# Kernel optimization log

Hardware: AMD Instinct MI355X
Metric: run time of the kernel (lower is better)

The kernel has to match this reference:

```python
import jax, jax.numpy as jnp
import numpy as np

E = 500000          # num edges
N = 50000           # num nodes
D_IN = 32           # n_input_features (edge feature dim)
D_HID = 128         # n_hidden_features
D_NODE = 16         # n_node_features; MLP head outputs D_NODE**2


def _linear_params(key, d_in, d_out):
    kw, kb = jax.random.split(key)
    bound = 1.0 / np.sqrt(d_in)
    W = jax.random.uniform(kw, (d_out, d_in), jnp.float32, -bound, bound)
    b = jax.random.uniform(kb, (d_out,), jnp.float32, -bound, bound)
    return W, b


def setup_inputs() -> dict:
    key = jax.random.key(0)
    k1, k2, k3, k4, k5, k6, k7 = jax.random.split(key, 7)
    edge_features = jax.random.normal(k1, (E, D_IN), jnp.float32)
    node_features = jax.random.normal(k2, (N, D_NODE), jnp.float32)
    edge_index = jax.random.randint(k3, (E, 2), 0, N, jnp.int64 if jax.config.jax_enable_x64 else jnp.int32)
    W1, b1 = _linear_params(k4, D_IN, D_HID)
    W2, b2 = _linear_params(k5, D_HID, D_HID)
    W3, b3 = _linear_params(k6, D_HID, D_HID)
    W4, b4 = _linear_params(k7, D_HID, D_NODE * D_NODE)
    return {
        "edge_features": edge_features,
        "node_features": node_features,
        "W1": W1, "b1": b1, "W2": W2, "b2": b2,
        "W3": W3, "b3": b3, "W4": W4, "b4": b4,
        "edge_index": edge_index,
    }


def reference(edge_features, node_features, W1, b1, W2, b2, W3, b3, W4, b4, edge_index):
    neighbors = edge_index[:, 1]                       # [E]
    ef = edge_features[neighbors]                      # [E, D_IN] gather
    nf = node_features[neighbors]                      # [E, D_NODE] gather
    h = jax.nn.relu(ef @ W1.T + b1)                    # [E, D_HID]
    h = jax.nn.relu(h @ W2.T + b2)
    h = jax.nn.relu(h @ W3.T + b3)
    edge_out = h @ W4.T + b4                           # [E, D_NODE**2]
    d = nf.shape[-1]
    message = edge_out.reshape(-1, d, d)               # [E, d, d]
    # per-edge matrix-vector product: (message @ nf[..., None]).squeeze(-1)
    return jnp.einsum("eij,ej->ei", message, nf)       # [E, d]
```

## Files before the change

kernel.cpp:

```cpp
#include <hip/hip_runtime.h>
#include <stdint.h>

typedef __attribute__((ext_vector_type(8))) short short8;
typedef __attribute__((ext_vector_type(4))) float f32x4;
typedef __attribute__((ext_vector_type(4))) unsigned int u32x4;

#define NE 500000
#define NN 50000
#define NTILES 3125
#define WSLOTS 2048
#define SC_BLOCKS 2048
#define SC_THREADS (SC_BLOCKS * 256)

__device__ __forceinline__ unsigned int f2bf1(float f) {
  unsigned int u = __builtin_bit_cast(unsigned int, f);
  u += 0x7FFFu + ((u >> 16) & 1u);
  return u >> 16;
}
__device__ __forceinline__ unsigned int packbf2(float lo, float hi) {
  return f2bf1(lo) | (f2bf1(hi) << 16);
}
__device__ __forceinline__ short8 pack8(f32x4 a, f32x4 b) {
  short8 r;
  r[0] = (short)f2bf1(a[0]); r[1] = (short)f2bf1(a[1]);
  r[2] = (short)f2bf1(a[2]); r[3] = (short)f2bf1(a[3]);
  r[4] = (short)f2bf1(b[0]); r[5] = (short)f2bf1(b[1]);
  r[6] = (short)f2bf1(b[2]); r[7] = (short)f2bf1(b[3]);
  return r;
}

__global__ __launch_bounds__(256) void prep_weights(
    const float* __restrict__ W1, const float* __restrict__ W2,
    const float* __restrict__ W3, const float* __restrict__ W4,
    unsigned short* __restrict__ wf) {
  int idx = blockIdx.x * 256 + threadIdx.x;
  if (idx >= 8704) return;
  int f = idx >> 6, l = idx & 63;
  int c2 = l & 15, g = l >> 4;
  const float *pa, *pb;
  if (f < 8) {
    const float* base = W1 + (f * 16 + c2) * 32 + g * 8;
    pa = base; pb = base + 4;
  } else {
    const float* W; int i2, kfq, nb;
    if (f < 40)      { W = W2; i2 = f - 8;  kfq = i2 >> 3; nb = i2 & 7;  }
    else if (f < 72) { W = W3; i2 = f - 40; kfq = i2 >> 3; nb = i2 & 7;  }
    else             { W = W4; i2 = f - 72; kfq = i2 >> 4; nb = i2 & 15; }
    const float* base = W + (nb * 16 + c2) * 128 + g * 4;
    pa = base + kfq * 16;
    pb = base + (kfq + 4) * 16;
  }
  f32x4 x0 = *(const f32x4*)pa;
  f32x4 x1 = *(const f32x4*)pb;
  *(short8*)&wf[f * 512 + l * 8] = pack8(x0, x1);
}

__global__ __launch_bounds__(512, 2) void mlp_kernel(
    const float* __restrict__ ef, const float* __restrict__ nfeat,
    const float* __restrict__ b1, const float* __restrict__ b2,
    const float* __restrict__ b3, const float* __restrict__ b4,
    const unsigned short* __restrict__ wf, float* __restrict__ Rout) {
  __shared__ __align__(16) unsigned short wlds[69632];
  __shared__ __align__(16) float blds[640];

  const int t = threadIdx.x;
  {
    const u32x4* src = (const u32x4*)wf;
    u32x4* dst = (u32x4*)wlds;
    #pragma unroll
    for (int i = 0; i < 17; ++i) dst[t + i * 512] = src[t + i * 512];
  }
  if (t < 160) {
    const float* s = t < 32 ? b1 + t * 4
                   : t < 64 ? b2 + (t - 32) * 4
                   : t < 96 ? b3 + (t - 64) * 4
                   :          b4 + (t - 96) * 4;
    ((f32x4*)blds)[t] = *(const f32x4*)s;
  }
  __syncthreads();

  const int lane = t & 63, w = t >> 6;
  const int l15 = lane & 15, lg = lane >> 4;

  const int g = w * 256 + blockIdx.x;
  const int tA = g;
  const bool actB = (g + WSLOTS < NTILES);
  const int tB = actB ? g + WSLOTS : g;
  const int nA = tA * 16, nB = tB * 16;

  auto transition = [&](const f32x4* a, short8* af) {
    unsigned int pk[8][2];
    #pragma unroll
    for (int nb = 0; nb < 8; ++nb) {
      pk[nb][0] = packbf2(fmaxf(a[nb][0], 0.f), fmaxf(a[nb][1], 0.f));
      pk[nb][1] = packbf2(fmaxf(a[nb][2], 0.f), fmaxf(a[nb][3], 0.f));
    }
    #pragma unroll
    for (int kf = 0; kf < 4; ++kf) {
      u32x4 u = { pk[kf][0], pk[kf][1], pk[kf + 4][0], pk[kf + 4][1] };
      af[kf] = __builtin_bit_cast(short8, u);
    }
  };

  const float* xa = ef + (nA + l15) * 32 + lg * 8;
  const float* xb = ef + (nB + l15) * 32 + lg * 8;
  short8 a1A = pack8(*(const f32x4*)xa, *(const f32x4*)(xa + 4));
  short8 a1B = pack8(*(const f32x4*)xb, *(const f32x4*)(xb + 4));
  f32x4 accA[8], accB[8];
  #pragma unroll
  for (int nb = 0; nb < 8; ++nb) {
    f32x4 c0 = *(const f32x4*)&blds[nb * 16 + lg * 4];
    short8 wv = *(const short8*)&wlds[nb * 512 + lane * 8];
    accA[nb] = __builtin_amdgcn_mfma_f32_16x16x32_bf16(wv, a1A, c0, 0, 0, 0);
    accB[nb] = __builtin_amdgcn_mfma_f32_16x16x32_bf16(wv, a1B, c0, 0, 0, 0);
  }
  short8 afA[4], afB[4];
  transition(accA, afA);
  transition(accB, afB);

  #pragma unroll
  for (int L = 0; L < 2; ++L) {
    const int wbase = 8 + L * 32, bbase = 128 + L * 128;
    #pragma unroll
    for (int nb = 0; nb < 8; ++nb) {
      f32x4 c0 = *(const f32x4*)&blds[bbase + nb * 16 + lg * 4];
      f32x4 cA = c0, cB = c0;
      #pragma unroll
      for (int kf = 0; kf < 4; ++kf) {
        short8 wv = *(const short8*)&wlds[(wbase + kf * 8 + nb) * 512 + lane * 8];
        cA = __builtin_amdgcn_mfma_f32_16x16x32_bf16(wv, afA[kf], cA, 0, 0, 0);
        cB = __builtin_amdgcn_mfma_f32_16x16x32_bf16(wv, afB[kf], cB, 0, 0, 0);
      }
      accA[nb] = cA; accB[nb] = cB;
    }
    transition(accA, afA);
    transition(accB, afB);
  }

  f32x4 nfvA = *(const f32x4*)(nfeat + (nA + l15) * 16 + lg * 4);
  f32x4 nfvB = *(const f32x4*)(nfeat + (nB + l15) * 16 + lg * 4);
  float oA0 = 0.f, oA1 = 0.f, oA2 = 0.f, oA3 = 0.f;
  float oB0 = 0.f, oB1 = 0.f, oB2 = 0.f, oB3 = 0.f;
  #pragma unroll
  for (int nb = 0; nb < 16; ++nb) {
    f32x4 c0 = *(const f32x4*)&blds[384 + nb * 16 + lg * 4];
    f32x4 dA = c0, dB = c0;
    #pragma unroll
    for (int kf = 0; kf < 4; ++kf) {
      short8 wv = *(const short8*)&wlds[(72 + kf * 16 + nb) * 512 + lane * 8];
      dA = __builtin_amdgcn_mfma_f32_16x16x32_bf16(wv, afA[kf], dA, 0, 0, 0);
      dB = __builtin_amdgcn_mfma_f32_16x16x32_bf16(wv, afB[kf], dB, 0, 0, 0);
    }
    float pA = dA[0]*nfvA[0] + dA[1]*nfvA[1] + dA[2]*nfvA[2] + dA[3]*nfvA[3];
    float pB = dB[0]*nfvB[0] + dB[1]*nfvB[1] + dB[2]*nfvB[2] + dB[3]*nfvB[3];
    pA += __shfl_xor(pA, 16, 64); pA += __shfl_xor(pA, 32, 64);
    pB += __shfl_xor(pB, 16, 64); pB += __shfl_xor(pB, 32, 64);
    int rs = nb - lg * 4;
    oA0 = (rs == 0) ? pA : oA0; oA1 = (rs == 1) ? pA : oA1;
    oA2 = (rs == 2) ? pA : oA2; oA3 = (rs == 3) ? pA : oA3;
    oB0 = (rs == 0) ? pB : oB0; oB1 = (rs == 1) ? pB : oB1;
    oB2 = (rs == 2) ? pB : oB2; oB3 = (rs == 3) ? pB : oB3;
  }
  f32x4 oA = { oA0, oA1, oA2, oA3 };
  *(f32x4*)(Rout + (nA + l15) * 16 + lg * 4) = oA;
  if (actB) {
    f32x4 oB = { oB0, oB1, oB2, oB3 };
    *(f32x4*)(Rout + (nB + l15) * 16 + lg * 4) = oB;
  }
}

__global__ __launch_bounds__(256) void scatter_kernel(
    const int* __restrict__ eidx, const float* __restrict__ Rbuf,
    float* __restrict__ out) {
  const int tid = blockIdx.x * 256 + threadIdx.x;
  const int total = NE * 4;
  const int i0 = tid;
  const int i1 = tid + SC_THREADS;
  const int i2 = tid + 2 * SC_THREADS;
  const int i3 = tid + 3 * SC_THREADS;
  const bool d3 = (i3 < total);

  int nA = eidx[((i0 >> 2) << 1) + 1];
  int nB = eidx[((i1 >> 2) << 1) + 1];
  int nC = eidx[((i2 >> 2) << 1) + 1];
  int nD = d3 ? eidx[((i3 >> 2) << 1) + 1] : 0;

  f32x4 vA = *(const f32x4*)(Rbuf + nA * 16 + (i0 & 3) * 4);
  f32x4 vB = *(const f32x4*)(Rbuf + nB * 16 + (i1 & 3) * 4);
  f32x4 vC = *(const f32x4*)(Rbuf + nC * 16 + (i2 & 3) * 4);
  f32x4 vD = d3 ? *(const f32x4*)(Rbuf + nD * 16 + (i3 & 3) * 4) : f32x4{0,0,0,0};

  *(f32x4*)(out + (size_t)i0 * 4) = vA;
  *(f32x4*)(out + (size_t)i1 * 4) = vB;
  *(f32x4*)(out + (size_t)i2 * 4) = vC;
  if (d3) *(f32x4*)(out + (size_t)i3 * 4) = vD;
}

extern "C" void kernel_launch(void* const* d_in, const int* in_sizes, int n_in,
                              void* d_out, int out_size, void* d_ws, size_t ws_size,
                              hipStream_t stream) {
  const float* ef = (const float*)d_in[0];
  const float* nf = (const float*)d_in[1];
  const float* W1 = (const float*)d_in[2];
  const float* b1 = (const float*)d_in[3];
  const float* W2 = (const float*)d_in[4];
  const float* b2 = (const float*)d_in[5];
  const float* W3 = (const float*)d_in[6];
  const float* b3 = (const float*)d_in[7];
  const float* W4 = (const float*)d_in[8];
  const float* b4 = (const float*)d_in[9];
  const int* eidx = (const int*)d_in[10];

  unsigned short* wfrag = (unsigned short*)d_ws;
  float* Rbuf = (float*)((char*)d_ws + 139264);
  float* out = (float*)d_out;

  hipLaunchKernelGGL(prep_weights, dim3(34), dim3(256), 0, stream,
                     W1, W2, W3, W4, wfrag);
  hipLaunchKernelGGL(mlp_kernel, dim3(256), dim3(512), 0, stream,
                     ef, nf, b1, b2, b3, b4, wfrag, Rbuf);
  hipLaunchKernelGGL(scatter_kernel, dim3(SC_BLOCKS), dim3(256), 0, stream,
                     eidx, Rbuf, out);
}
```

Baseline: 36.94 us.

## Shrink MLP LDS footprint, one tile per wave, read W4 from global

The MLP kernel no longer stages the W4 fragments in LDS. Those are now read straight from global memory (L2-cached), which roughly halves shared memory per block. Each wave processes one 16-node tile instead of two, the grid grows to 391 blocks, and launch bounds ask for 4 blocks per CU to raise occupancy. The edge-feature load is hoisted above the weight copy so it overlaps the LDS staging. The trade-off is losing the two-tile interleaving that hid MFMA latency, and W4 global loads inside the final layer loop may add latency.

```diff
diff --git a/kernel.cpp b/kernel.cpp
--- a/kernel.cpp
+++ b/kernel.cpp
@@ -8,7 +8,7 @@
 #define NE 500000
 #define NN 50000
 #define NTILES 3125
-#define WSLOTS 2048
+#define MLP_BLOCKS 391
 #define SC_BLOCKS 2048
 #define SC_THREADS (SC_BLOCKS * 256)
 
@@ -55,20 +55,29 @@
   *(short8*)&wf[f * 512 + l * 8] = pack8(x0, x1);
 }
 
-__global__ __launch_bounds__(512, 2) void mlp_kernel(
+__global__ __launch_bounds__(512, 4) void mlp_kernel(
     const float* __restrict__ ef, const float* __restrict__ nfeat,
     const float* __restrict__ b1, const float* __restrict__ b2,
     const float* __restrict__ b3, const float* __restrict__ b4,
     const unsigned short* __restrict__ wf, float* __restrict__ Rout) {
-  __shared__ __align__(16) unsigned short wlds[69632];
+  __shared__ __align__(16) unsigned short wlds[36864];
   __shared__ __align__(16) float blds[640];
 
   const int t = threadIdx.x;
+  const int lane = t & 63, w = t >> 6;
+  const int l15 = lane & 15, lg = lane >> 4;
+  const int tile = blockIdx.x * 8 + w;
+  const int n0 = (tile < NTILES ? tile : 0) * 16;
+
+  const float* xp = ef + (n0 + l15) * 32 + lg * 8;
+  f32x4 x0 = *(const f32x4*)xp;
+  f32x4 x1 = *(const f32x4*)(xp + 4);
+
   {
     const u32x4* src = (const u32x4*)wf;
     u32x4* dst = (u32x4*)wlds;
     #pragma unroll
-    for (int i = 0; i < 17; ++i) dst[t + i * 512] = src[t + i * 512];
+    for (int i = 0; i < 9; ++i) dst[t + i * 512] = src[t + i * 512];
   }
   if (t < 160) {
     const float* s = t < 32 ? b1 + t * 4
@@ -79,14 +88,7 @@
   }
   __syncthreads();
 
-  const int lane = t & 63, w = t >> 6;
-  const int l15 = lane & 15, lg = lane >> 4;
-
-  const int g = w * 256 + blockIdx.x;
-  const int tA = g;
-  const bool actB = (g + WSLOTS < NTILES);
-  const int tB = actB ? g + WSLOTS : g;
-  const int nA = tA * 16, nB = tB * 16;
+  if (tile >= NTILES) return;
 
   auto transition = [&](const f32x4* a, short8* af) {
     unsigned int pk[8][2];
@@ -102,71 +104,53 @@
     }
   };
 
-  const float* xa = ef + (nA + l15) * 32 + lg * 8;
-  const float* xb = ef + (nB + l15) * 32 + lg * 8;
-  short8 a1A = pack8(*(const f32x4*)xa, *(const f32x4*)(xa + 4));
-  short8 a1B = pack8(*(const f32x4*)xb, *(const f32x4*)(xb + 4));
-  f32x4 accA[8], accB[8];
+  short8 a1 = pack8(x0, x1);
+  f32x4 acc[8];
   #pragma unroll
   for (int nb = 0; nb < 8; ++nb) {
     f32x4 c0 = *(const f32x4*)&blds[nb * 16 + lg * 4];
     short8 wv = *(const short8*)&wlds[nb * 512 + lane * 8];
-    accA[nb] = __builtin_amdgcn_mfma_f32_16x16x32_bf16(wv, a1A, c0, 0, 0, 0);
-    accB[nb] = __builtin_amdgcn_mfma_f32_16x16x32_bf16(wv, a1B, c0, 0, 0, 0);
-  }
-  short8 afA[4], afB[4];
-  transition(accA, afA);
-  transition(accB, afB);
+    acc[nb] = __builtin_amdgcn_mfma_f32_16x16x32_bf16(wv, a1, c0, 0, 0, 0);
+  }
+  short8 af[4];
+  transition(acc, af);
 
   #pragma unroll
   for (int L = 0; L < 2; ++L) {
     const int wbase = 8 + L * 32, bbase = 128 + L * 128;
     #pragma unroll
     for (int nb = 0; nb < 8; ++nb) {
-      f32x4 c0 = *(const f32x4*)&blds[bbase + nb * 16 + lg * 4];
-      f32x4 cA = c0, cB = c0;
+      f32x4 c = *(const f32x4*)&blds[bbase + nb * 16 + lg * 4];
       #pragma unroll
       for (int kf = 0; kf < 4; ++kf) {
         short8 wv = *(const short8*)&wlds[(wbase + kf * 8 + nb) * 512 + lane * 8];
-        cA = __builtin_amdgcn_mfma_f32_16x16x32_bf16(wv, afA[kf], cA, 0, 0, 0);
-        cB = __builtin_amdgcn_mfma_f32_16x16x32_bf16(wv, afB[kf], cB, 0, 0, 0);
+        c = __builtin_amdgcn_mfma_f32_16x16x32_bf16(wv, af[kf], c, 0, 0, 0);
       }
-      accA[nb] = cA; accB[nb] = cB;
-    }
-    transition(accA, afA);
-    transition(accB, afB);
-  }
-
-  f32x4 nfvA = *(const f32x4*)(nfeat + (nA + l15) * 16 + lg * 4);
-  f32x4 nfvB = *(const f32x4*)(nfeat + (nB + l15) * 16 + lg * 4);
-  float oA0 = 0.f, oA1 = 0.f, oA2 = 0.f, oA3 = 0.f;
-  float oB0 = 0.f, oB1 = 0.f, oB2 = 0.f, oB3 = 0.f;
+      acc[nb] = c;
+    }
+    transition(acc, af);
+  }
+
+  const short8* w4 = (const short8*)(wf + 72 * 512);
+  f32x4 nfv = *(const f32x4*)(nfeat + (n0 + l15) * 16 + lg * 4);
+  float o0 = 0.f, o1 = 0.f, o2 = 0.f, o3 = 0.f;
   #pragma unroll
   for (int nb = 0; nb < 16; ++nb) {
-    f32x4 c0 = *(const f32x4*)&blds[384 + nb * 16 + lg * 4];
-    f32x4 dA = c0, dB = c0;
+    f32x4 d = *(const f32x4*)&blds[384 + nb * 16 + lg * 4];
     #pragma unroll
     for (int kf = 0; kf < 4; ++kf) {
-      short8 wv = *(const short8*)&wlds[(72 + kf * 16 + nb) * 512 + lane * 8];
-      dA = __builtin_amdgcn_mfma_f32_16x16x32_bf16(wv, afA[kf], dA, 0, 0, 0);
-      dB = __builtin_amdgcn_mfma_f32_16x16x32_bf16(wv, afB[kf], dB, 0, 0, 0);
-    }
-    float pA = dA[0]*nfvA[0] + dA[1]*nfvA[1] + dA[2]*nfvA[2] + dA[3]*nfvA[3];
-    float pB = dB[0]*nfvB[0] + dB[1]*nfvB[1] + dB[2]*nfvB[2] + dB[3]*nfvB[3];
-    pA += __shfl_xor(pA, 16, 64); pA += __shfl_xor(pA, 32, 64);
-    pB += __shfl_xor(pB, 16, 64); pB += __shfl_xor(pB, 32, 64);
+      short8 wv = w4[(kf * 16 + nb) * 64 + lane];
+      d = __builtin_amdgcn_mfma_f32_16x16x32_bf16(wv, af[kf], d, 0, 0, 0);
+    }
+    float p = d[0]*nfv[0] + d[1]*nfv[1] + d[2]*nfv[2] + d[3]*nfv[3];
+    p += __shfl_xor(p, 16, 64);
+    p += __shfl_xor(p, 32, 64);
     int rs = nb - lg * 4;
-    oA0 = (rs == 0) ? pA : oA0; oA1 = (rs == 1) ? pA : oA1;
-    oA2 = (rs == 2) ? pA : oA2; oA3 = (rs == 3) ? pA : oA3;
-    oB0 = (rs == 0) ? pB : oB0; oB1 = (rs == 1) ? pB : oB1;
-    oB2 = (rs == 2) ? pB : oB2; oB3 = (rs == 3) ? pB : oB3;
-  }
-  f32x4 oA = { oA0, oA1, oA2, oA3 };
-  *(f32x4*)(Rout + (nA + l15) * 16 + lg * 4) = oA;
-  if (actB) {
-    f32x4 oB = { oB0, oB1, oB2, oB3 };
-    *(f32x4*)(Rout + (nB + l15) * 16 + lg * 4) = oB;
-  }
+    o0 = (rs == 0) ? p : o0; o1 = (rs == 1) ? p : o1;
+    o2 = (rs == 2) ? p : o2; o3 = (rs == 3) ? p : o3;
+  }
+  f32x4 o = { o0, o1, o2, o3 };
+  *(f32x4*)(Rout + (n0 + l15) * 16 + lg * 4) = o;
 }
 
 __global__ __launch_bounds__(256) void scatter_kernel(
@@ -217,7 +201,7 @@
 
   hipLaunchKernelGGL(prep_weights, dim3(34), dim3(256), 0, stream,
                      W1, W2, W3, W4, wfrag);
-  hipLaunchKernelGGL(mlp_kernel, dim3(256), dim3(512), 0, stream,
+  hipLaunchKernelGGL(mlp_kernel, dim3(MLP_BLOCKS), dim3(512), 0, stream,
                      ef, nf, b1, b2, b3, b4, wfrag, Rbuf);
   hipLaunchKernelGGL(scatter_kernel, dim3(SC_BLOCKS), dim3(256), 0, stream,
                      eidx, Rbuf, out);
```

After: 38.07 us. 1.03x slower.
